# Kernel optimization log

Hardware: AMD Instinct MI355X
Metric: run time of the kernel (lower is better)

## Reference

```python
import jax, jax.numpy as jnp
import numpy as np


def setup_inputs() -> dict:
    key = jax.random.key(0)
    ks = jax.random.split(key, 12)
    B, Nv, C, H, W = 4, 4096, 64, 376, 1240
    inp = {
        "voxel_features": jax.random.normal(ks[0], (B, Nv, C), jnp.float32),
        "voxels_3d": jax.random.normal(ks[1], (B, Nv, 3), jnp.float32),
        "img_feats": jax.random.normal(ks[2], (B, C, H, W), jnp.float32),
        "vox_x": jax.random.randint(ks[3], (B, Nv), 0, 1400, jnp.int32),
        "vox_y": jax.random.randint(ks[4], (B, Nv), 0, 430, jnp.int32),
        "q_w": jax.random.normal(ks[5], (C, C), jnp.float32) / np.sqrt(C),
        "q_b": jnp.zeros((C,), jnp.float32),
        "k_w": jax.random.normal(ks[6], (C, 3), jnp.float32) / np.sqrt(3.0),
        "k_b": jnp.zeros((C,), jnp.float32),
        "v_w": jax.random.normal(ks[7], (C, C), jnp.float32) / np.sqrt(C),
        "v_b": jnp.zeros((C,), jnp.float32),
        "o_w": jax.random.normal(ks[8], (C, C), jnp.float32) / np.sqrt(C),
        "o_b": jnp.zeros((C,), jnp.float32),
        "fc_w": jax.random.normal(ks[9], (C, C), jnp.float32) / np.sqrt(C),
    }
    return inp


def reference(voxel_features, voxels_3d, img_feats, vox_x, vox_y,
              q_w, q_b, k_w, k_b, v_w, v_b, o_w, o_b, fc_w):
    # voxel_features: [B, Nv, C] lidar voxel features (value)
    # voxels_3d:      [B, Nv, 3] voxel 3D coords (key)
    # img_feats:      [B, C, H, W] image feature map
    B, C, H, W = img_feats.shape
    Nv = voxel_features.shape[1]

    # --- gather image features at projected voxel pixel coords, zero if OOB ---
    valid = (vox_x >= 0) & (vox_x < W) & (vox_y >= 0) & (vox_y < H)  # [B, Nv]
    xc = jnp.clip(vox_x, 0, W - 1)
    yc = jnp.clip(vox_y, 0, H - 1)
    b_idx = jnp.arange(B)[:, None]
    camera = img_feats[b_idx, :, yc, xc]            # [B, Nv, C]
    camera = jnp.where(valid[..., None], camera, 0.0)

    # --- single-head cross-modal attention (q=camera, k=coords, v=lidar) ---
    scale = 1.0 / jnp.sqrt(jnp.asarray(C, camera.dtype))
    q = (camera @ q_w.T + q_b) * scale              # [B, Nv, C]
    k = voxels_3d @ k_w.T + k_b                     # [B, Nv, C]
    v = voxel_features @ v_w.T + v_b                # [B, Nv, C]
    scores = jnp.einsum('bqc,bkc->bqk', q, k)       # [B, Nv, Nv]
    attn = jax.nn.softmax(scores, axis=-1)
    ctx = jnp.einsum('bqk,bkc->bqc', attn, v)
    ctx = ctx @ o_w.T + o_b                         # out_proj

    fused = jax.nn.relu(ctx @ fc_w.T)               # [B, Nv, C]
    return jnp.concatenate([voxel_features, fused], axis=-1)  # [B, Nv, 2C]
```

## Files before the change

kernel.cpp:

```cpp
#include <hip/hip_runtime.h>

#define BB 4
#define NV 4096
#define BN (BB * NV)
#define CC 64
#define HH 376
#define WW 1240
#define HW (HH * WW)
#define LDT 72
#define LDK 36
#define NSPLIT 8
#define TILES 8
#define QSCALE 0.1803368801111244f

typedef __bf16 bf16x8 __attribute__((ext_vector_type(8)));
typedef __bf16 bf16x4 __attribute__((ext_vector_type(4)));
typedef float  f32x4  __attribute__((ext_vector_type(4)));

__global__ __launch_bounds__(256) void kprep(
    const float* __restrict__ vfeat, const float* __restrict__ v3d,
    const float* __restrict__ img, const int* __restrict__ vx,
    const int* __restrict__ vy, const float* __restrict__ qw,
    const float* __restrict__ qb, const float* __restrict__ kwm,
    const float* __restrict__ vw, const float* __restrict__ vb,
    float* __restrict__ out, unsigned short* __restrict__ Qp,
    unsigned short* __restrict__ K32, unsigned short* __restrict__ VTb) {
  __shared__ float VfS[32][68];
  __shared__ float CamS[32][68];
  __shared__ float WqkS[64][4];
  __shared__ float bqkS[4];
  const int tid = threadIdx.x;
  const int vl = tid >> 3;
  const int p = tid & 7;
  const int gv = blockIdx.x * 32 + vl;
  const int b = gv >> 12, n = gv & (NV - 1);
  const size_t row = (size_t)b * NV + n;

  if (tid < 192) {
    int j = tid / 3, d = tid - j * 3;
    float a = 0.f;
    for (int c = 0; c < CC; ++c) a = fmaf(qw[c * CC + j], kwm[c * 3 + d], a);
    WqkS[j][d] = a;
  } else if (tid < 195) {
    int d = tid - 192;
    float a = 0.f;
    for (int c = 0; c < CC; ++c) a = fmaf(qb[c], kwm[c * 3 + d], a);
    bqkS[d] = a;
  }

  {
    const float4* vf4 = (const float4*)(vfeat + row * CC) + p * 2;
    float4* o4 = (float4*)(out + row * 128) + p * 2;
    float4* s4 = (float4*)&VfS[vl][p * 8];
#pragma unroll
    for (int i = 0; i < 2; ++i) { float4 t = vf4[i]; o4[i] = t; s4[i] = t; }
  }

  {
    int x = vx[row], y = vy[row];
    bool valid = (x >= 0) & (x < WW) & (y >= 0) & (y < HH);
    int xs = valid ? x : 0, ys = valid ? y : 0;
    const float* ib = img + ((size_t)b * CC + p * 8) * (size_t)HW + (size_t)ys * WW + xs;
#pragma unroll
    for (int i = 0; i < 8; ++i) {
      float cv = ib[(size_t)i * HW];
      CamS[vl][p * 8 + i] = valid ? cv : 0.f;
    }
  }

  if (p == 0) {
    float c0 = v3d[row * 3 + 0], c1 = v3d[row * 3 + 1], c2 = v3d[row * 3 + 2];
    bf16x8 kp = {(__bf16)c0, (__bf16)c1, (__bf16)c2, (__bf16)0.f,
                 (__bf16)0.f, (__bf16)0.f, (__bf16)0.f, (__bf16)0.f};
    *(bf16x8*)(K32 + row * 32) = kp;
  } else if (p < 4) {
    bf16x8 z = {(__bf16)0.f, (__bf16)0.f, (__bf16)0.f, (__bf16)0.f,
                (__bf16)0.f, (__bf16)0.f, (__bf16)0.f, (__bf16)0.f};
    *(bf16x8*)(K32 + row * 32 + p * 8) = z;
  }
  __syncthreads();

  {
    f32x4 vr[16];
#pragma unroll
    for (int i = 0; i < 16; ++i) vr[i] = *(const f32x4*)&VfS[vl][i * 4];
#pragma unroll
    for (int cc = 0; cc < 8; ++cc) {
      int c = p * 8 + cc;
      const float4* w4 = (const float4*)(vw + c * CC);
      float acc = vb[c];
#pragma unroll
      for (int j = 0; j < 16; ++j) {
        float4 w = w4[j];
        acc = fmaf(vr[j][0], w.x, fmaf(vr[j][1], w.y, fmaf(vr[j][2], w.z, fmaf(vr[j][3], w.w, acc))));
      }
      ((__bf16*)VTb)[((size_t)b * CC + c) * NV + n] = (__bf16)acc;
    }
  }

  if (p == 0) {
    float q0 = bqkS[0], q1 = bqkS[1], q2 = bqkS[2];
#pragma unroll 8
    for (int j = 0; j < CC; ++j) {
      float c = CamS[vl][j];
      q0 = fmaf(c, WqkS[j][0], q0);
      q1 = fmaf(c, WqkS[j][1], q1);
      q2 = fmaf(c, WqkS[j][2], q2);
    }
    bf16x8 qp = {(__bf16)(q0 * QSCALE), (__bf16)(q1 * QSCALE), (__bf16)(q2 * QSCALE),
                 (__bf16)0.f, (__bf16)0.f, (__bf16)0.f, (__bf16)0.f, (__bf16)0.f};
    *(bf16x8*)(Qp + row * 32) = qp;
  } else if (p < 4) {
    bf16x8 z = {(__bf16)0.f, (__bf16)0.f, (__bf16)0.f, (__bf16)0.f,
                (__bf16)0.f, (__bf16)0.f, (__bf16)0.f, (__bf16)0.f};
    *(bf16x8*)(Qp + row * 32 + p * 8) = z;
  }
}

__global__ __launch_bounds__(256, 3) void kattn(const unsigned short* __restrict__ Qp,
                                                const unsigned short* __restrict__ K32,
                                                const unsigned short* __restrict__ VTb,
                                                unsigned short* __restrict__ Opb,
                                                float* __restrict__ ml) {
  __shared__ unsigned short Ks[2][64 * LDK];
  __shared__ unsigned short Vs[2][64 * LDT];
  __shared__ unsigned short Ps[4][2][16 * LDT];

  const int bid = blockIdx.x;
  const int xcd = bid & 7;
  const int idx = bid >> 3;
  const int combo = xcd * 4 + (idx >> 5);
  const int qc = idx & 31;
  const int b = combo >> 3;
  const int sp = combo & 7;
  const int q0 = qc * 128;
  const int key0 = sp * (TILES * 64);

  const int tid = threadIdx.x;
  const int wid = tid >> 6;
  const int lane = tid & 63;
  const int lq = lane & 15;
  const int lg = lane >> 4;

  const int srow = tid >> 2;
  const int scol = (tid & 3) * 16;
  const int kcol = (tid & 3) * 8;

  const size_t qrow = (size_t)b * NV + q0 + wid * 32 + lq;
  bf16x8 qf0 = *(const bf16x8*)(Qp + qrow * 32 + lg * 8);
  bf16x8 qf1 = *(const bf16x8*)(Qp + (qrow + 16) * 32 + lg * 8);

  const f32x4 cinit = {-16.f, -16.f, -16.f, -16.f};
  float l0 = 0.f, l1 = 0.f;
  f32x4 oacc0[4], oacc1[4];
#pragma unroll
  for (int t = 0; t < 4; ++t) { oacc0[t] = {0.f, 0.f, 0.f, 0.f}; oacc1[t] = {0.f, 0.f, 0.f, 0.f}; }

  const unsigned short* kgb = K32 + ((size_t)b * NV) * 32;
  const unsigned short* vgb = VTb + (size_t)b * CC * NV;

  uint4 kq, vr0, vr1;
  {
    kq = *(const uint4*)(kgb + (size_t)(key0 + srow) * 32 + kcol);
    const uint4* vsrc = (const uint4*)(vgb + (size_t)srow * NV + key0 + scol);
    vr0 = vsrc[0]; vr1 = vsrc[1];
    *(uint4*)&Ks[0][srow * LDK + kcol] = kq;
    uint4* vdst = (uint4*)&Vs[0][srow * LDT + scol];
    vdst[0] = vr0; vdst[1] = vr1;
  }
  __syncthreads();

  int cur = 0;
  for (int tt = 0; tt < TILES; ++tt) {
    if (tt + 1 < TILES) {
      int k0 = key0 + (tt + 1) * 64;
      kq = *(const uint4*)(kgb + (size_t)(k0 + srow) * 32 + kcol);
      const uint4* vsrc = (const uint4*)(vgb + (size_t)srow * NV + k0 + scol);
      vr0 = vsrc[0]; vr1 = vsrc[1];
    }

#pragma unroll
    for (int t = 0; t < 4; ++t) {
      bf16x8 ka = *(const bf16x8*)&Ks[cur][(t * 16 + lq) * LDK + lg * 8];
      f32x4 s0 = __builtin_amdgcn_mfma_f32_16x16x32_bf16(ka, qf0, cinit, 0, 0, 0);
      f32x4 s1 = __builtin_amdgcn_mfma_f32_16x16x32_bf16(ka, qf1, cinit, 0, 0, 0);
      float a0 = __builtin_amdgcn_exp2f(s0[0]);
      float a1 = __builtin_amdgcn_exp2f(s0[1]);
      float a2 = __builtin_amdgcn_exp2f(s0[2]);
      float a3 = __builtin_amdgcn_exp2f(s0[3]);
      l0 += (a0 + a1) + (a2 + a3);
      bf16x4 pk0;
      pk0[0] = (__bf16)a0; pk0[1] = (__bf16)a1; pk0[2] = (__bf16)a2; pk0[3] = (__bf16)a3;
      *(bf16x4*)&Ps[wid][0][lq * LDT + t * 16 + lg * 4] = pk0;
      float c0 = __builtin_amdgcn_exp2f(s1[0]);
      float c1 = __builtin_amdgcn_exp2f(s1[1]);
      float c2 = __builtin_amdgcn_exp2f(s1[2]);
      float c3 = __builtin_amdgcn_exp2f(s1[3]);
      l1 += (c0 + c1) + (c2 + c3);
      bf16x4 pk1;
      pk1[0] = (__bf16)c0; pk1[1] = (__bf16)c1; pk1[2] = (__bf16)c2; pk1[3] = (__bf16)c3;
      *(bf16x4*)&Ps[wid][1][lq * LDT + t * 16 + lg * 4] = pk1;
    }

#pragma unroll
    for (int ks = 0; ks < 2; ++ks) {
      bf16x8 pa0 = *(const bf16x8*)&Ps[wid][0][lq * LDT + ks * 32 + lg * 8];
      bf16x8 pa1 = *(const bf16x8*)&Ps[wid][1][lq * LDT + ks * 32 + lg * 8];
#pragma unroll
      for (int t = 0; t < 4; ++t) {
        bf16x8 vbf = *(const bf16x8*)&Vs[cur][(t * 16 + lq) * LDT + ks * 32 + lg * 8];
        oacc0[t] = __builtin_amdgcn_mfma_f32_16x16x32_bf16(pa0, vbf, oacc0[t], 0, 0, 0);
        oacc1[t] = __builtin_amdgcn_mfma_f32_16x16x32_bf16(pa1, vbf, oacc1[t], 0, 0, 0);
      }
    }

    if (tt + 1 < TILES) {
      *(uint4*)&Ks[cur ^ 1][srow * LDK + kcol] = kq;
      uint4* vdst = (uint4*)&Vs[cur ^ 1][srow * LDT + scol];
      vdst[0] = vr0; vdst[1] = vr1;
    }
    __syncthreads();
    cur ^= 1;
  }

  l0 += __shfl_xor(l0, 16); l0 += __shfl_xor(l0, 32);
  l1 += __shfl_xor(l1, 16); l1 += __shfl_xor(l1, 32);

  const size_t obase = (size_t)sp * BN + (size_t)b * NV + q0 + wid * 32;
#pragma unroll
  for (int r = 0; r < 4; ++r) {
    __bf16* op0 = (__bf16*)Opb + (obase + lg * 4 + r) * CC + lq;
    __bf16* op1 = (__bf16*)Opb + (obase + 16 + lg * 4 + r) * CC + lq;
#pragma unroll
    for (int t = 0; t < 4; ++t) {
      op0[t * 16] = (__bf16)oacc0[t][r];
      op1[t * 16] = (__bf16)oacc1[t][r];
    }
  }
  if (lg == 0) {
    ml[obase + lq] = l0;
    ml[obase + 16 + lq] = l1;
  }
}

__global__ __launch_bounds__(256) void kmerge(const unsigned short* __restrict__ Opb,
                                              const float* __restrict__ ml,
                                              const float* __restrict__ ow,
                                              const float* __restrict__ ob,
                                              const float* __restrict__ fc,
                                              float* __restrict__ out) {
  __shared__ unsigned short W2s[64 * LDT];
  __shared__ float b2s[64];
  const int tid = threadIdx.x;
  const int wid = tid >> 6;
  const int lane = tid & 63;
  const int lq = lane & 15;
  const int lg = lane >> 4;

  {
    const int i = tid >> 2;
    const int jb = (tid & 3) * 16;
    float acc[16];
#pragma unroll
    for (int e = 0; e < 16; ++e) acc[e] = 0.f;
    for (int k = 0; k < CC; ++k) {
      float f = fc[i * CC + k];
      const float4* o4 = (const float4*)(ow + k * CC + jb);
#pragma unroll
      for (int e4 = 0; e4 < 4; ++e4) {
        float4 o = o4[e4];
        acc[e4 * 4 + 0] = fmaf(f, o.x, acc[e4 * 4 + 0]);
        acc[e4 * 4 + 1] = fmaf(f, o.y, acc[e4 * 4 + 1]);
        acc[e4 * 4 + 2] = fmaf(f, o.z, acc[e4 * 4 + 2]);
        acc[e4 * 4 + 3] = fmaf(f, o.w, acc[e4 * 4 + 3]);
      }
    }
    __bf16* wrow = (__bf16*)&W2s[i * LDT + jb];
#pragma unroll
    for (int e = 0; e < 16; ++e) wrow[e] = (__bf16)acc[e];
    if (tid < CC) {
      float a = 0.f;
      for (int k = 0; k < CC; ++k) a = fmaf(fc[tid * CC + k], ob[k], a);
      b2s[tid] = a;
    }
  }
  __syncthreads();

  const int row = blockIdx.x * 64 + wid * 16 + lq;

  float lstar = 0.f;
#pragma unroll
  for (int s = 0; s < NSPLIT; ++s) lstar += ml[(size_t)s * BN + row];

  float ctx[16];
#pragma unroll
  for (int j = 0; j < 16; ++j) ctx[j] = 0.f;
#pragma unroll
  for (int s = 0; s < NSPLIT; ++s) {
    const __bf16* oprow = (const __bf16*)Opb + ((size_t)s * BN + row) * CC;
    bf16x8 a0 = *(const bf16x8*)(oprow + lg * 8);
    bf16x8 a1 = *(const bf16x8*)(oprow + 32 + lg * 8);
#pragma unroll
    for (int j = 0; j < 8; ++j) {
      ctx[j] += (float)a0[j];
      ctx[8 + j] += (float)a1[j];
    }
  }
  float inv = 1.f / lstar;
  bf16x8 cb0, cb1;
#pragma unroll
  for (int j = 0; j < 8; ++j) {
    cb0[j] = (__bf16)(ctx[j] * inv);
    cb1[j] = (__bf16)(ctx[8 + j] * inv);
  }

  const f32x4 vzero = {0.f, 0.f, 0.f, 0.f};
  float* orow = out + (size_t)row * 128 + 64;
#pragma unroll
  for (int t2 = 0; t2 < 4; ++t2) {
    bf16x8 wa0 = *(const bf16x8*)&W2s[(t2 * 16 + lq) * LDT + lg * 8];
    bf16x8 wa1 = *(const bf16x8*)&W2s[(t2 * 16 + lq) * LDT + 32 + lg * 8];
    f32x4 r2 = vzero;
    r2 = __builtin_amdgcn_mfma_f32_16x16x32_bf16(wa0, cb0, r2, 0, 0, 0);
    r2 = __builtin_amdgcn_mfma_f32_16x16x32_bf16(wa1, cb1, r2, 0, 0, 0);
    float4 o;
    o.x = fmaxf(r2[0] + b2s[t2 * 16 + lg * 4 + 0], 0.f);
    o.y = fmaxf(r2[1] + b2s[t2 * 16 + lg * 4 + 1], 0.f);
    o.z = fmaxf(r2[2] + b2s[t2 * 16 + lg * 4 + 2], 0.f);
    o.w = fmaxf(r2[3] + b2s[t2 * 16 + lg * 4 + 3], 0.f);
    *(float4*)(orow + t2 * 16 + lg * 4) = o;
  }
}

extern "C" void kernel_launch(void* const* d_in, const int* in_sizes, int n_in,
                              void* d_out, int out_size, void* d_ws, size_t ws_size,
                              hipStream_t stream) {
  const float* vfeat = (const float*)d_in[0];
  const float* v3d = (const float*)d_in[1];
  const float* img = (const float*)d_in[2];
  const int* vx = (const int*)d_in[3];
  const int* vy = (const int*)d_in[4];
  const float* qw = (const float*)d_in[5];
  const float* qb = (const float*)d_in[6];
  const float* kwm = (const float*)d_in[7];
  const float* vw = (const float*)d_in[9];
  const float* vb = (const float*)d_in[10];
  const float* ow = (const float*)d_in[11];
  const float* ob = (const float*)d_in[12];
  const float* fc = (const float*)d_in[13];
  float* out = (float*)d_out;

  char* ws = (char*)d_ws;
  unsigned short* Qp = (unsigned short*)(ws);
  unsigned short* K32 = (unsigned short*)(ws + (1u << 20));
  unsigned short* VTb = (unsigned short*)(ws + (2u << 20));
  unsigned short* Opb = (unsigned short*)(ws + (4u << 20));
  float* ml = (float*)(ws + (20u << 20));

  kprep<<<512, 256, 0, stream>>>(vfeat, v3d, img, vx, vy, qw, qb, kwm, vw, vb,
                                 out, Qp, K32, VTb);
  kattn<<<1024, 256, 0, stream>>>(Qp, K32, VTb, Opb, ml);
  kmerge<<<256, 256, 0, stream>>>(Opb, ml, ow, ob, fc, out);
}
```

Measured before the change: 98.90 us.

## Fuse split-K merge into attention kernel via last-block atomic counter

Drops the separate merge kernel. The last of the split blocks for each query chunk, found with an atomic counter, does the reduction, output projection and ReLU. The split count falls from 8 to 4 with twice as many key tiles per block, and the folded fc·o weight is precomputed in the prep kernel. Partial outputs are now staged through LDS so global stores are coalesced. This removes a kernel launch and the weight folding done in every merge block, at the cost of half the grid size (512 blocks), lower occupancy bounds, and a serial tail in the last-arriving blocks.

```diff
diff --git a/kernel.cpp b/kernel.cpp
--- a/kernel.cpp
+++ b/kernel.cpp
@@ -9,8 +9,8 @@
 #define HW (HH * WW)
 #define LDT 72
 #define LDK 36
-#define NSPLIT 8
-#define TILES 8
+#define NSPLIT 4
+#define TILES 16
 #define QSCALE 0.1803368801111244f
 
 typedef __bf16 bf16x8 __attribute__((ext_vector_type(8)));
@@ -23,8 +23,12 @@
     const int* __restrict__ vy, const float* __restrict__ qw,
     const float* __restrict__ qb, const float* __restrict__ kwm,
     const float* __restrict__ vw, const float* __restrict__ vb,
+    const float* __restrict__ ow, const float* __restrict__ ob,
+    const float* __restrict__ fc,
     float* __restrict__ out, unsigned short* __restrict__ Qp,
-    unsigned short* __restrict__ K32, unsigned short* __restrict__ VTb) {
+    unsigned short* __restrict__ K32, unsigned short* __restrict__ VTb,
+    int* __restrict__ cnt, unsigned short* __restrict__ W2b,
+    float* __restrict__ b2f) {
   __shared__ float VfS[32][68];
   __shared__ float CamS[32][68];
   __shared__ float WqkS[64][4];
@@ -36,6 +40,26 @@
   const int b = gv >> 12, n = gv & (NV - 1);
   const size_t row = (size_t)b * NV + n;
 
+  if (blockIdx.x < 128 && tid == 0) cnt[blockIdx.x] = 0;
+
+  if (blockIdx.x < 4) {
+    const int i = blockIdx.x * 16 + (tid >> 4);
+    const int jb = (tid & 15) * 4;
+    float a0 = 0.f, a1 = 0.f, a2 = 0.f, a3 = 0.f;
+    for (int k = 0; k < CC; ++k) {
+      float f = fc[i * CC + k];
+      const float4 o = *(const float4*)(ow + k * CC + jb);
+      a0 = fmaf(f, o.x, a0); a1 = fmaf(f, o.y, a1);
+      a2 = fmaf(f, o.z, a2); a3 = fmaf(f, o.w, a3);
+    }
+    bf16x4 wv; wv[0] = (__bf16)a0; wv[1] = (__bf16)a1; wv[2] = (__bf16)a2; wv[3] = (__bf16)a3;
+    *(bf16x4*)(W2b + i * CC + jb) = wv;
+  } else if (blockIdx.x == 4 && tid < CC) {
+    float a = 0.f;
+    for (int k = 0; k < CC; ++k) a = fmaf(fc[tid * CC + k], ob[k], a);
+    b2f[tid] = a;
+  }
+
   if (tid < 192) {
     int j = tid / 3, d = tid - j * 3;
     float a = 0.f;
@@ -117,22 +141,27 @@
   }
 }
 
-__global__ __launch_bounds__(256, 3) void kattn(const unsigned short* __restrict__ Qp,
+__global__ __launch_bounds__(256, 2) void kattn(const unsigned short* __restrict__ Qp,
                                                 const unsigned short* __restrict__ K32,
                                                 const unsigned short* __restrict__ VTb,
                                                 unsigned short* __restrict__ Opb,
-                                                float* __restrict__ ml) {
+                                                float* __restrict__ ml,
+                                                int* __restrict__ cnt,
+                                                const unsigned short* __restrict__ W2b,
+                                                const float* __restrict__ b2f,
+                                                float* __restrict__ out) {
   __shared__ unsigned short Ks[2][64 * LDK];
   __shared__ unsigned short Vs[2][64 * LDT];
   __shared__ unsigned short Ps[4][2][16 * LDT];
+  __shared__ int lastFlag;
 
   const int bid = blockIdx.x;
   const int xcd = bid & 7;
   const int idx = bid >> 3;
-  const int combo = xcd * 4 + (idx >> 5);
+  const int combo = xcd * 2 + (idx >> 5);
   const int qc = idx & 31;
-  const int b = combo >> 3;
-  const int sp = combo & 7;
+  const int b = combo >> 2;
+  const int sp = combo & 3;
   const int q0 = qc * 128;
   const int key0 = sp * (TILES * 64);
 
@@ -226,109 +255,99 @@
   l0 += __shfl_xor(l0, 16); l0 += __shfl_xor(l0, 32);
   l1 += __shfl_xor(l1, 16); l1 += __shfl_xor(l1, 32);
 
-  const size_t obase = (size_t)sp * BN + (size_t)b * NV + q0 + wid * 32;
-#pragma unroll
-  for (int r = 0; r < 4; ++r) {
-    __bf16* op0 = (__bf16*)Opb + (obase + lg * 4 + r) * CC + lq;
-    __bf16* op1 = (__bf16*)Opb + (obase + 16 + lg * 4 + r) * CC + lq;
-#pragma unroll
-    for (int t = 0; t < 4; ++t) {
-      op0[t * 16] = (__bf16)oacc0[t][r];
-      op1[t * 16] = (__bf16)oacc1[t][r];
-    }
-  }
-  if (lg == 0) {
-    ml[obase + lq] = l0;
-    ml[obase + 16 + lq] = l1;
-  }
-}
-
-__global__ __launch_bounds__(256) void kmerge(const unsigned short* __restrict__ Opb,
-                                              const float* __restrict__ ml,
-                                              const float* __restrict__ ow,
-                                              const float* __restrict__ ob,
-                                              const float* __restrict__ fc,
-                                              float* __restrict__ out) {
-  __shared__ unsigned short W2s[64 * LDT];
-  __shared__ float b2s[64];
-  const int tid = threadIdx.x;
-  const int wid = tid >> 6;
-  const int lane = tid & 63;
-  const int lq = lane & 15;
-  const int lg = lane >> 4;
-
-  {
-    const int i = tid >> 2;
-    const int jb = (tid & 3) * 16;
-    float acc[16];
-#pragma unroll
-    for (int e = 0; e < 16; ++e) acc[e] = 0.f;
-    for (int k = 0; k < CC; ++k) {
-      float f = fc[i * CC + k];
-      const float4* o4 = (const float4*)(ow + k * CC + jb);
-#pragma unroll
-      for (int e4 = 0; e4 < 4; ++e4) {
-        float4 o = o4[e4];
-        acc[e4 * 4 + 0] = fmaf(f, o.x, acc[e4 * 4 + 0]);
-        acc[e4 * 4 + 1] = fmaf(f, o.y, acc[e4 * 4 + 1]);
-        acc[e4 * 4 + 2] = fmaf(f, o.z, acc[e4 * 4 + 2]);
-        acc[e4 * 4 + 3] = fmaf(f, o.w, acc[e4 * 4 + 3]);
+  {
+    unsigned short* myVs = (unsigned short*)Vs + wid * (32 * 68);
+#pragma unroll
+    for (int r = 0; r < 4; ++r) {
+#pragma unroll
+      for (int t = 0; t < 4; ++t) {
+        ((__bf16*)myVs)[(lg * 4 + r) * 68 + t * 16 + lq] = (__bf16)oacc0[t][r];
+        ((__bf16*)myVs)[(16 + lg * 4 + r) * 68 + t * 16 + lq] = (__bf16)oacc1[t][r];
       }
     }
-    __bf16* wrow = (__bf16*)&W2s[i * LDT + jb];
-#pragma unroll
-    for (int e = 0; e < 16; ++e) wrow[e] = (__bf16)acc[e];
-    if (tid < CC) {
-      float a = 0.f;
-      for (int k = 0; k < CC; ++k) a = fmaf(fc[tid * CC + k], ob[k], a);
-      b2s[tid] = a;
-    }
+    const int rq = lane & 31, hf = lane >> 5;
+    const unsigned short* src = &myVs[rq * 68 + hf * 32];
+    uint4 w0 = *(const uint4*)(src);
+    uint4 w1 = *(const uint4*)(src + 8);
+    uint4 w2 = *(const uint4*)(src + 16);
+    uint4 w3 = *(const uint4*)(src + 24);
+    const size_t obase = (size_t)sp * BN + (size_t)b * NV + q0 + wid * 32;
+    unsigned short* oprow = Opb + (obase + rq) * CC + hf * 32;
+    *(uint4*)(oprow) = w0;
+    *(uint4*)(oprow + 8) = w1;
+    *(uint4*)(oprow + 16) = w2;
+    *(uint4*)(oprow + 24) = w3;
+    if (lg == 0) {
+      ml[obase + lq] = l0;
+      ml[obase + 16 + lq] = l1;
+    }
+  }
+
+  __threadfence();
+  if (tid == 0) {
+    int old = atomicAdd(&cnt[b * 32 + qc], 1);
+    lastFlag = (old == NSPLIT - 1);
   }
   __syncthreads();
-
-  const int row = blockIdx.x * 64 + wid * 16 + lq;
-
-  float lstar = 0.f;
-#pragma unroll
-  for (int s = 0; s < NSPLIT; ++s) lstar += ml[(size_t)s * BN + row];
-
-  float ctx[16];
-#pragma unroll
-  for (int j = 0; j < 16; ++j) ctx[j] = 0.f;
-#pragma unroll
-  for (int s = 0; s < NSPLIT; ++s) {
-    const __bf16* oprow = (const __bf16*)Opb + ((size_t)s * BN + row) * CC;
-    bf16x8 a0 = *(const bf16x8*)(oprow + lg * 8);
-    bf16x8 a1 = *(const bf16x8*)(oprow + 32 + lg * 8);
+  if (!lastFlag) return;
+  __threadfence();
+
+  unsigned short* W2s = (unsigned short*)Ps;
+  float* b2s = (float*)Ks;
+  {
+    const uint4* wsrc = (const uint4*)(W2b + srow * CC + scol);
+    uint4* wd = (uint4*)&W2s[srow * LDT + scol];
+    wd[0] = wsrc[0]; wd[1] = wsrc[1];
+    if (tid < CC) b2s[tid] = b2f[tid];
+  }
+  __syncthreads();
+
+  const f32x4 vzero = {0.f, 0.f, 0.f, 0.f};
+#pragma unroll
+  for (int half = 0; half < 2; ++half) {
+    const int row = b * NV + q0 + half * 64 + wid * 16 + lq;
+
+    float lstar = 0.f;
+#pragma unroll
+    for (int s = 0; s < NSPLIT; ++s) lstar += ml[(size_t)s * BN + row];
+
+    float ctx[16];
+#pragma unroll
+    for (int j = 0; j < 16; ++j) ctx[j] = 0.f;
+#pragma unroll
+    for (int s = 0; s < NSPLIT; ++s) {
+      const __bf16* oprow = (const __bf16*)Opb + ((size_t)s * BN + row) * CC;
+      bf16x8 a0 = *(const bf16x8*)(oprow + lg * 8);
+      bf16x8 a1 = *(const bf16x8*)(oprow + 32 + lg * 8);
+#pragma unroll
+      for (int j = 0; j < 8; ++j) {
+        ctx[j] += (float)a0[j];
+        ctx[8 + j] += (float)a1[j];
+      }
+    }
+    float inv = 1.f / lstar;
+    bf16x8 cb0, cb1;
 #pragma unroll
     for (int j = 0; j < 8; ++j) {
-      ctx[j] += (float)a0[j];
-      ctx[8 + j] += (float)a1[j];
-    }
-  }
-  float inv = 1.f / lstar;
-  bf16x8 cb0, cb1;
-#pragma unroll
-  for (int j = 0; j < 8; ++j) {
-    cb0[j] = (__bf16)(ctx[j] * inv);
-    cb1[j] = (__bf16)(ctx[8 + j] * inv);
-  }
-
-  const f32x4 vzero = {0.f, 0.f, 0.f, 0.f};
-  float* orow = out + (size_t)row * 128 + 64;
-#pragma unroll
-  for (int t2 = 0; t2 < 4; ++t2) {
-    bf16x8 wa0 = *(const bf16x8*)&W2s[(t2 * 16 + lq) * LDT + lg * 8];
-    bf16x8 wa1 = *(const bf16x8*)&W2s[(t2 * 16 + lq) * LDT + 32 + lg * 8];
-    f32x4 r2 = vzero;
-    r2 = __builtin_amdgcn_mfma_f32_16x16x32_bf16(wa0, cb0, r2, 0, 0, 0);
-    r2 = __builtin_amdgcn_mfma_f32_16x16x32_bf16(wa1, cb1, r2, 0, 0, 0);
-    float4 o;
-    o.x = fmaxf(r2[0] + b2s[t2 * 16 + lg * 4 + 0], 0.f);
-    o.y = fmaxf(r2[1] + b2s[t2 * 16 + lg * 4 + 1], 0.f);
-    o.z = fmaxf(r2[2] + b2s[t2 * 16 + lg * 4 + 2], 0.f);
-    o.w = fmaxf(r2[3] + b2s[t2 * 16 + lg * 4 + 3], 0.f);
-    *(float4*)(orow + t2 * 16 + lg * 4) = o;
+      cb0[j] = (__bf16)(ctx[j] * inv);
+      cb1[j] = (__bf16)(ctx[8 + j] * inv);
+    }
+
+    float* orow = out + (size_t)row * 128 + 64;
+#pragma unroll
+    for (int t2 = 0; t2 < 4; ++t2) {
+      bf16x8 wa0 = *(const bf16x8*)&W2s[(t2 * 16 + lq) * LDT + lg * 8];
+      bf16x8 wa1 = *(const bf16x8*)&W2s[(t2 * 16 + lq) * LDT + 32 + lg * 8];
+      f32x4 r2 = vzero;
+      r2 = __builtin_amdgcn_mfma_f32_16x16x32_bf16(wa0, cb0, r2, 0, 0, 0);
+      r2 = __builtin_amdgcn_mfma_f32_16x16x32_bf16(wa1, cb1, r2, 0, 0, 0);
+      float4 o;
+      o.x = fmaxf(r2[0] + b2s[t2 * 16 + lg * 4 + 0], 0.f);
+      o.y = fmaxf(r2[1] + b2s[t2 * 16 + lg * 4 + 1], 0.f);
+      o.z = fmaxf(r2[2] + b2s[t2 * 16 + lg * 4 + 2], 0.f);
+      o.w = fmaxf(r2[3] + b2s[t2 * 16 + lg * 4 + 3], 0.f);
+      *(float4*)(orow + t2 * 16 + lg * 4) = o;
+    }
   }
 }
 
@@ -355,10 +374,12 @@
   unsigned short* K32 = (unsigned short*)(ws + (1u << 20));
   unsigned short* VTb = (unsigned short*)(ws + (2u << 20));
   unsigned short* Opb = (unsigned short*)(ws + (4u << 20));
-  float* ml = (float*)(ws + (20u << 20));
+  float* ml = (float*)(ws + (12u << 20));
+  int* cnt = (int*)(ws + (12u << 20) + (256u << 10));
+  unsigned short* W2b = (unsigned short*)(ws + (12u << 20) + (256u << 10) + 1024);
+  float* b2f = (float*)(ws + (12u << 20) + (256u << 10) + 1024 + 8192);
 
   kprep<<<512, 256, 0, stream>>>(vfeat, v3d, img, vx, vy, qw, qb, kwm, vw, vb,
-                                 out, Qp, K32, VTb);
-  kattn<<<1024, 256, 0, stream>>>(Qp, K32, VTb, Opb, ml);
-  kmerge<<<256, 256, 0, stream>>>(Opb, ml, ow, ob, fc, out);
+                                 ow, ob, fc, out, Qp, K32, VTb, cnt, W2b, b2f);
+  kattn<<<512, 256, 0, stream>>>(Qp, K32, VTb, Opb, ml, cnt, W2b, b2f, out);
 }
```

Measured after the change: 160.2 us. 1.62x slower.
